# Optimization experiments

Hardware: AMD Instinct MI355X
Metric: run time of the kernel (lower is better)

## Reference

```python
import jax, jax.numpy as jnp
import numpy as np

N_EMBED = 512  # c in the original; scale uses sqrt(c), not head_size


def setup_inputs() -> dict:
    key = jax.random.key(0)
    k1, k2, k3, k4 = jax.random.split(key, 4)
    B, T, C, H = 4, 4096, N_EMBED, 64
    x = jax.random.normal(k1, (B, T, C), dtype=jnp.float32)
    Wk = jax.random.normal(k2, (C, H), dtype=jnp.float32) * (1.0 / np.sqrt(C))
    Wq = jax.random.normal(k3, (C, H), dtype=jnp.float32) * (1.0 / np.sqrt(C))
    Wv = jax.random.normal(k4, (C, H), dtype=jnp.float32) * (1.0 / np.sqrt(C))
    return {"x": x, "Wk": Wk, "Wq": Wq, "Wv": Wv}


def reference(x, Wk, Wq, Wv):
    # x: [B, T, C]; Wk/Wq/Wv: [C, H]
    B, T, C = x.shape
    k = jnp.einsum('btc,ch->bth', x, Wk)
    q = jnp.einsum('btc,ch->bth', x, Wq)
    v = jnp.einsum('btc,ch->bth', x, Wv)
    scale = 1.0 / jnp.sqrt(jnp.float32(C))  # original divides by sqrt(c)
    scores = jnp.einsum('bth,bsh->bts', q, k) * scale  # [B, T, T]
    causal = jnp.tril(jnp.ones((T, T), dtype=bool))
    scores = jnp.where(causal, scores, -jnp.inf)
    attn = jax.nn.softmax(scores, axis=-1)
    # dropout = 0.0 -> identity
    out = jnp.einsum('bts,bsh->bth', attn, v)  # [B, T, H]
    return out
```

## Files before the change

kernel.cpp:

```cpp
#include <hip/hip_runtime.h>
#include <hip/hip_bf16.h>
#include <math.h>

#define NB 4
#define NT 4096
#define NC 512
#define NH 64
#define KVBLK 64
#define LDK 72
#define MASKV (-1e30f)

typedef __attribute__((ext_vector_type(8))) short bf16x8;
typedef __attribute__((ext_vector_type(4))) float f32x4;

__device__ inline unsigned short f2bf(float f) {
    __hip_bfloat16 h = __float2bfloat16(f);
    return *reinterpret_cast<unsigned short*>(&h);
}

__global__ __launch_bounds__(256) void wconv(
    const float* __restrict__ Wk, const float* __restrict__ Wq,
    const float* __restrict__ Wv, unsigned short* __restrict__ Wt)
{
    int idx = blockIdx.x * 256 + threadIdx.x;
    int n = idx % 192, c = idx / 192;
    int sel = n >> 6, h = n & 63;
    const float* W = (sel == 0) ? Wq : (sel == 1) ? Wk : Wv;
    float val = W[c * NH + h];
    if (sel == 0) val *= 0.044194173824159216f;
    Wt[n * NC + c] = f2bf(val);
}

__global__ __launch_bounds__(256) void qkv_gemm(
    const float* __restrict__ x, const unsigned short* __restrict__ Wt,
    unsigned short* __restrict__ q, unsigned short* __restrict__ k,
    unsigned short* __restrict__ vt)
{
    __shared__ unsigned short xa[32][LDK];
    __shared__ unsigned short wb[192][LDK];

    const int tid = threadIdx.x;
    const int w = tid >> 6, lane = tid & 63, l15 = lane & 15, g = lane >> 4;
    const size_t r0 = (size_t)blockIdx.x * 32;

    f32x4 acc[2][3];
    #pragma unroll
    for (int mt = 0; mt < 2; ++mt)
        #pragma unroll
        for (int nt = 0; nt < 3; ++nt) acc[mt][nt] = (f32x4){0.f,0.f,0.f,0.f};

    for (int c0 = 0; c0 < NC; c0 += 64) {
        __syncthreads();
        {
            int row = tid >> 3, f8 = tid & 7;
            const float* xp = x + (r0 + row) * NC + c0 + f8*8;
            float4 x0 = *reinterpret_cast<const float4*>(xp);
            float4 x1 = *reinterpret_cast<const float4*>(xp + 4);
            bf16x8 a8;
            a8[0]=f2bf(x0.x); a8[1]=f2bf(x0.y); a8[2]=f2bf(x0.z); a8[3]=f2bf(x0.w);
            a8[4]=f2bf(x1.x); a8[5]=f2bf(x1.y); a8[6]=f2bf(x1.z); a8[7]=f2bf(x1.w);
            *reinterpret_cast<bf16x8*>(&xa[row][f8*8]) = a8;
        }
        #pragma unroll
        for (int i = 0; i < 6; ++i) {
            int idx = tid + 256*i;
            int row = idx >> 3, f8 = idx & 7;
            bf16x8 w8 = *reinterpret_cast<const bf16x8*>(Wt + (size_t)row * NC + c0 + f8*8);
            *reinterpret_cast<bf16x8*>(&wb[row][f8*8]) = w8;
        }
        __syncthreads();

        #pragma unroll
        for (int kk = 0; kk < 2; ++kk) {
            bf16x8 a[2], bfr[3];
            #pragma unroll
            for (int mt = 0; mt < 2; ++mt)
                a[mt] = *reinterpret_cast<const bf16x8*>(&xa[16*mt + l15][32*kk + 8*g]);
            #pragma unroll
            for (int nt = 0; nt < 3; ++nt)
                bfr[nt] = *reinterpret_cast<const bf16x8*>(&wb[48*w + 16*nt + l15][32*kk + 8*g]);
            __builtin_amdgcn_s_setprio(1);
            #pragma unroll
            for (int mt = 0; mt < 2; ++mt)
                #pragma unroll
                for (int nt = 0; nt < 3; ++nt)
                    acc[mt][nt] = __builtin_amdgcn_mfma_f32_16x16x32_bf16(a[mt], bfr[nt], acc[mt][nt], 0, 0, 0);
            __builtin_amdgcn_s_setprio(0);
        }
    }

    #pragma unroll
    for (int mt = 0; mt < 2; ++mt)
        #pragma unroll
        for (int nt = 0; nt < 3; ++nt) {
            int ncol = 48*w + 16*nt + l15;
            int sel = ncol >> 6, h = ncol & 63;
            if (sel < 2) {
                unsigned short* dst = (sel == 0) ? q : k;
                #pragma unroll
                for (int r = 0; r < 4; ++r)
                    dst[(r0 + 16*mt + 4*g + r) * NH + h] = f2bf(acc[mt][nt][r]);
            } else {
                int bb = (int)(r0 >> 12);
                int trow = ((int)r0 & (NT-1)) + 16*mt + 4*g;
                unsigned int lo = (unsigned int)f2bf(acc[mt][nt][0]) | ((unsigned int)f2bf(acc[mt][nt][1]) << 16);
                unsigned int hi = (unsigned int)f2bf(acc[mt][nt][2]) | ((unsigned int)f2bf(acc[mt][nt][3]) << 16);
                *reinterpret_cast<uint2*>(&vt[((size_t)bb*NH + h)*NT + trow]) = make_uint2(lo, hi);
            }
        }
}

__global__ __launch_bounds__(64, 3) void attn_part(
    const unsigned short* __restrict__ qg,
    const unsigned short* __restrict__ kg,
    const unsigned short* __restrict__ vtg,
    float* __restrict__ out,
    float* __restrict__ O_part,
    float* __restrict__ ML_part)
{
    const int qt = 127 - blockIdx.x;
    const int nT = (qt >> 1) + 1;
    const int ch = blockIdx.y;
    if (8 * ch >= nT) return;
    const int b  = blockIdx.z;

    __shared__ unsigned short p_lds[32][LDK];

    const int lane = threadIdx.x & 63;
    const int l15  = lane & 15;
    const int g    = lane >> 4;

    const int q0 = qt * 32;
    const size_t base = (size_t)b * NT * NH;

    bf16x8 qf[2][2];
    #pragma unroll
    for (int qc = 0; qc < 2; ++qc) {
        const unsigned short* qp = qg + base + (size_t)(q0 + 16*qc + l15) * NH + 8*g;
        qf[qc][0] = *reinterpret_cast<const bf16x8*>(qp);
        qf[qc][1] = *reinterpret_cast<const bf16x8*>(qp + 32);
    }

    f32x4 ot[4][2];
    #pragma unroll
    for (int dt = 0; dt < 4; ++dt)
        #pragma unroll
        for (int qc = 0; qc < 2; ++qc) ot[dt][qc] = (f32x4){0.f,0.f,0.f,0.f};
    float m0 = MASKV, m1 = MASKV, l0 = 0.f, l1 = 0.f;

    const int tBeg = 8 * ch;
    const int tEnd = min(8 * (ch + 1), nT);

    for (int it = tBeg; it < tEnd; ++it) {
        const int s0 = it * KVBLK;

        const unsigned short* kbase = kg + base + (size_t)(s0 + l15) * NH + 8*g;
        bf16x8 ka[4][2];
        #pragma unroll
        for (int t = 0; t < 4; ++t)
            #pragma unroll
            for (int kk = 0; kk < 2; ++kk)
                ka[t][kk] = *reinterpret_cast<const bf16x8*>(kbase + t*16*NH + kk*32);

        f32x4 s[4][2];
        __builtin_amdgcn_s_setprio(1);
        #pragma unroll
        for (int t = 0; t < 4; ++t)
            #pragma unroll
            for (int qc = 0; qc < 2; ++qc) {
                s[t][qc] = __builtin_amdgcn_mfma_f32_16x16x32_bf16(ka[t][0], qf[qc][0], (f32x4){0.f,0.f,0.f,0.f}, 0, 0, 0);
                s[t][qc] = __builtin_amdgcn_mfma_f32_16x16x32_bf16(ka[t][1], qf[qc][1], s[t][qc], 0, 0, 0);
            }
        __builtin_amdgcn_s_setprio(0);

        const unsigned short* vbase = vtg + ((size_t)b*NH + l15)*NT + s0 + 8*g;
        bf16x8 vf[4][2];
        #pragma unroll
        for (int dt = 0; dt < 4; ++dt)
            #pragma unroll
            for (int kk = 0; kk < 2; ++kk)
                vf[dt][kk] = *reinterpret_cast<const bf16x8*>(vbase + (size_t)dt*16*NT + kk*32);

        if (s0 + KVBLK - 1 > q0) {
            #pragma unroll
            for (int t = 0; t < 4; ++t)
                #pragma unroll
                for (int qc = 0; qc < 2; ++qc) {
                    const int qr = q0 + 16*qc + l15;
                    #pragma unroll
                    for (int r = 0; r < 4; ++r)
                        if (s0 + 16*t + 4*g + r > qr) s[t][qc][r] = MASKV;
                }
        }

        float pm0 = MASKV, pm1 = MASKV;
        #pragma unroll
        for (int t = 0; t < 4; ++t)
            #pragma unroll
            for (int r = 0; r < 4; ++r) {
                pm0 = fmaxf(pm0, s[t][0][r]);
                pm1 = fmaxf(pm1, s[t][1][r]);
            }
        pm0 = fmaxf(pm0, __shfl_xor(pm0, 16)); pm0 = fmaxf(pm0, __shfl_xor(pm0, 32));
        pm1 = fmaxf(pm1, __shfl_xor(pm1, 16)); pm1 = fmaxf(pm1, __shfl_xor(pm1, 32));

        if (!__all(pm0 <= m0 + 8.f && pm1 <= m1 + 8.f)) {
            float mn0 = fmaxf(m0, pm0), mn1 = fmaxf(m1, pm1);
            float c0 = __expf(m0 - mn0), c1 = __expf(m1 - mn1);
            l0 *= c0; l1 *= c1;
            #pragma unroll
            for (int dt = 0; dt < 4; ++dt)
                #pragma unroll
                for (int e = 0; e < 4; ++e) {
                    ot[dt][0][e] *= c0;
                    ot[dt][1][e] *= c1;
                }
            m0 = mn0; m1 = mn1;
        }

        float ps0 = 0.f, ps1 = 0.f;
        #pragma unroll
        for (int t = 0; t < 4; ++t)
            #pragma unroll
            for (int r = 0; r < 4; ++r) {
                float p0 = __expf(s[t][0][r] - m0);
                float p1 = __expf(s[t][1][r] - m1);
                s[t][0][r] = p0; s[t][1][r] = p1;
                ps0 += p0; ps1 += p1;
            }

        #pragma unroll
        for (int qc = 0; qc < 2; ++qc)
            #pragma unroll
            for (int t = 0; t < 4; ++t) {
                unsigned int w0 = (unsigned int)f2bf(s[t][qc][0]) | ((unsigned int)f2bf(s[t][qc][1]) << 16);
                unsigned int w1 = (unsigned int)f2bf(s[t][qc][2]) | ((unsigned int)f2bf(s[t][qc][3]) << 16);
                *reinterpret_cast<unsigned int*>(&p_lds[16*qc + l15][16*t + 4*g])     = w0;
                *reinterpret_cast<unsigned int*>(&p_lds[16*qc + l15][16*t + 4*g + 2]) = w1;
            }

        ps0 += __shfl_xor(ps0, 16); ps0 += __shfl_xor(ps0, 32);
        ps1 += __shfl_xor(ps1, 16); ps1 += __shfl_xor(ps1, 32);
        l0 += ps0; l1 += ps1;

        bf16x8 pf[2][2];
        #pragma unroll
        for (int qc = 0; qc < 2; ++qc)
            #pragma unroll
            for (int kk = 0; kk < 2; ++kk)
                pf[qc][kk] = *reinterpret_cast<const bf16x8*>(&p_lds[16*qc + l15][8*g + 32*kk]);
        __builtin_amdgcn_s_setprio(1);
        #pragma unroll
        for (int kk = 0; kk < 2; ++kk)
            #pragma unroll
            for (int dt = 0; dt < 4; ++dt)
                #pragma unroll
                for (int qc = 0; qc < 2; ++qc)
                    ot[dt][qc] = __builtin_amdgcn_mfma_f32_16x16x32_bf16(vf[dt][kk], pf[qc][kk], ot[dt][qc], 0, 0, 0);
        __builtin_amdgcn_s_setprio(0);
    }

    if (nT <= 8) {
        const float inv0 = 1.f / l0, inv1 = 1.f / l1;
        #pragma unroll
        for (int qc = 0; qc < 2; ++qc) {
            float inv = qc ? inv1 : inv0;
            float* orow = out + base + (size_t)(q0 + 16*qc + l15) * NH;
            #pragma unroll
            for (int dt = 0; dt < 4; ++dt) {
                f32x4 o4;
                #pragma unroll
                for (int r = 0; r < 4; ++r) o4[r] = ot[dt][qc][r] * inv;
                *reinterpret_cast<f32x4*>(&orow[16*dt + 4*g]) = o4;
            }
        }
    } else {
        const int slot = ((b * 128 + qt) << 3) + ch;
        float* op = O_part + (size_t)slot * (32*NH);
        #pragma unroll
        for (int qc = 0; qc < 2; ++qc)
            #pragma unroll
            for (int dt = 0; dt < 4; ++dt)
                *reinterpret_cast<f32x4*>(&op[(size_t)(16*qc + l15) * NH + 16*dt + 4*g]) = ot[dt][qc];
        if (g == 0) {
            float* mlp = ML_part + (size_t)slot * 64;
            *reinterpret_cast<float2*>(&mlp[2*l15])        = make_float2(m0, l0);
            *reinterpret_cast<float2*>(&mlp[2*(16 + l15)]) = make_float2(m1, l1);
        }
    }
}

__global__ __launch_bounds__(256) void attn_merge(
    const float* __restrict__ O_part,
    const float* __restrict__ ML_part,
    float* __restrict__ out)
{
    const int qt = 16 + blockIdx.x;
    const int b  = blockIdx.y;
    const int nch = (((qt >> 1) + 1) + 7) >> 3;
    const int slot0 = ((b * 128 + qt) << 3);
    const int row = threadIdx.x >> 3;
    const int dq  = (threadIdx.x & 7) * 8;

    float M = MASKV;
    for (int c = 0; c < nch; ++c)
        M = fmaxf(M, ML_part[(size_t)(slot0 + c) * 64 + 2*row]);

    float L = 0.f;
    float acc[8];
    #pragma unroll
    for (int j = 0; j < 8; ++j) acc[j] = 0.f;

    for (int c = 0; c < nch; ++c) {
        const float* mlp = &ML_part[(size_t)(slot0 + c) * 64 + 2*row];
        float wgt = __expf(mlp[0] - M);
        L += wgt * mlp[1];
        const float* op = O_part + (size_t)(slot0 + c) * (32*NH) + (size_t)row * NH + dq;
        #pragma unroll
        for (int j4 = 0; j4 < 2; ++j4) {
            float4 o4 = *reinterpret_cast<const float4*>(op + 4*j4);
            acc[4*j4+0] = fmaf(wgt, o4.x, acc[4*j4+0]);
            acc[4*j4+1] = fmaf(wgt, o4.y, acc[4*j4+1]);
            acc[4*j4+2] = fmaf(wgt, o4.z, acc[4*j4+2]);
            acc[4*j4+3] = fmaf(wgt, o4.w, acc[4*j4+3]);
        }
    }

    const float inv = 1.f / L;
    float* orow = out + (size_t)b * NT * NH + (size_t)(qt * 32 + row) * NH + dq;
    #pragma unroll
    for (int j4 = 0; j4 < 2; ++j4) {
        float4 o4;
        o4.x = acc[4*j4+0] * inv;
        o4.y = acc[4*j4+1] * inv;
        o4.z = acc[4*j4+2] * inv;
        o4.w = acc[4*j4+3] * inv;
        *reinterpret_cast<float4*>(orow + 4*j4) = o4;
    }
}

extern "C" void kernel_launch(void* const* d_in, const int* in_sizes, int n_in,
                              void* d_out, int out_size, void* d_ws, size_t ws_size,
                              hipStream_t stream) {
    const float* x  = (const float*)d_in[0];
    const float* Wk = (const float*)d_in[1];
    const float* Wq = (const float*)d_in[2];
    const float* Wv = (const float*)d_in[3];
    float* out = (float*)d_out;

    const size_t n = (size_t)NB * NT * NH;
    unsigned short* qb = (unsigned short*)d_ws;
    unsigned short* kb = qb + n;
    unsigned short* vt = kb + n;
    unsigned short* Wt = vt + n;
    float* O_part  = (float*)(Wt + 192 * NC);
    float* ML_part = O_part + (size_t)4096 * 32 * NH;

    wconv<<<(192*NC)/256, 256, 0, stream>>>(Wk, Wq, Wv, Wt);
    qkv_gemm<<<(NB*NT)/32, 256, 0, stream>>>(x, Wt, qb, kb, vt);

    dim3 pgrid(128, 8, NB);
    attn_part<<<pgrid, 64, 0, stream>>>(qb, kb, vt, out, O_part, ML_part);
    dim3 mgrid(112, NB);
    attn_merge<<<mgrid, 256, 0, stream>>>(O_part, ML_part, out);
}
```

Baseline: 73.76 us.

## Split KV into finer chunks, pack four waves per block, store bf16 partials

The KV range per split shrinks from 8 tiles to 4, and four independent wave-level work items are packed into each 256-thread block, so the work is spread across more waves with better occupancy. The softmax switches to exp2f, with log2(e) folded into the Q scaling. Partial outputs are stored as bf16 instead of fp32 to cut merge-pass traffic. The cost is more partials to merge and reduced precision in the partial accumulators. Waves whose chunk index is out of range exit early, which leaves some lanes in a block idle.

```diff
diff --git a/kernel.cpp b/kernel.cpp
--- a/kernel.cpp
+++ b/kernel.cpp
@@ -9,6 +9,7 @@
 #define KVBLK 64
 #define LDK 72
 #define MASKV (-1e30f)
+#define CHT 4
 
 typedef __attribute__((ext_vector_type(8))) short bf16x8;
 typedef __attribute__((ext_vector_type(4))) float f32x4;
@@ -16,6 +17,10 @@
 __device__ inline unsigned short f2bf(float f) {
     __hip_bfloat16 h = __float2bfloat16(f);
     return *reinterpret_cast<unsigned short*>(&h);
+}
+__device__ inline float bf2f(unsigned int u16bits) {
+    unsigned int u = u16bits << 16;
+    return *reinterpret_cast<float*>(&u);
 }
 
 __global__ __launch_bounds__(256) void wconv(
@@ -27,7 +32,7 @@
     int sel = n >> 6, h = n & 63;
     const float* W = (sel == 0) ? Wq : (sel == 1) ? Wk : Wv;
     float val = W[c * NH + h];
-    if (sel == 0) val *= 0.044194173824159216f;
+    if (sel == 0) val *= 0.063758715f;
     Wt[n * NC + c] = f2bf(val);
 }
 
@@ -110,26 +115,27 @@
         }
 }
 
-__global__ __launch_bounds__(64, 3) void attn_part(
+__global__ __launch_bounds__(256, 4) void attn_part(
     const unsigned short* __restrict__ qg,
     const unsigned short* __restrict__ kg,
     const unsigned short* __restrict__ vtg,
     float* __restrict__ out,
-    float* __restrict__ O_part,
+    unsigned short* __restrict__ O_part,
     float* __restrict__ ML_part)
 {
-    const int qt = 127 - blockIdx.x;
+    __shared__ unsigned short p_lds[4][32][LDK];
+
+    const int w    = threadIdx.x >> 6;
+    const int lane = threadIdx.x & 63;
+    const int linear = blockIdx.x * 4 + w;
+    const int ch = linear & 15;
+    const int qt = 127 - (linear >> 4);
     const int nT = (qt >> 1) + 1;
-    const int ch = blockIdx.y;
-    if (8 * ch >= nT) return;
-    const int b  = blockIdx.z;
-
-    __shared__ unsigned short p_lds[32][LDK];
-
-    const int lane = threadIdx.x & 63;
+    if (CHT * ch >= nT) return;
+    const int b  = blockIdx.y;
+
     const int l15  = lane & 15;
     const int g    = lane >> 4;
-
     const int q0 = qt * 32;
     const size_t base = (size_t)b * NT * NH;
 
@@ -148,8 +154,8 @@
         for (int qc = 0; qc < 2; ++qc) ot[dt][qc] = (f32x4){0.f,0.f,0.f,0.f};
     float m0 = MASKV, m1 = MASKV, l0 = 0.f, l1 = 0.f;
 
-    const int tBeg = 8 * ch;
-    const int tEnd = min(8 * (ch + 1), nT);
+    const int tBeg = CHT * ch;
+    const int tEnd = min(CHT * (ch + 1), nT);
 
     for (int it = tBeg; it < tEnd; ++it) {
         const int s0 = it * KVBLK;
@@ -206,7 +212,7 @@
 
         if (!__all(pm0 <= m0 + 8.f && pm1 <= m1 + 8.f)) {
             float mn0 = fmaxf(m0, pm0), mn1 = fmaxf(m1, pm1);
-            float c0 = __expf(m0 - mn0), c1 = __expf(m1 - mn1);
+            float c0 = exp2f(m0 - mn0), c1 = exp2f(m1 - mn1);
             l0 *= c0; l1 *= c1;
             #pragma unroll
             for (int dt = 0; dt < 4; ++dt)
@@ -223,8 +229,8 @@
         for (int t = 0; t < 4; ++t)
             #pragma unroll
             for (int r = 0; r < 4; ++r) {
-                float p0 = __expf(s[t][0][r] - m0);
-                float p1 = __expf(s[t][1][r] - m1);
+                float p0 = exp2f(s[t][0][r] - m0);
+                float p1 = exp2f(s[t][1][r] - m1);
                 s[t][0][r] = p0; s[t][1][r] = p1;
                 ps0 += p0; ps1 += p1;
             }
@@ -235,8 +241,8 @@
             for (int t = 0; t < 4; ++t) {
                 unsigned int w0 = (unsigned int)f2bf(s[t][qc][0]) | ((unsigned int)f2bf(s[t][qc][1]) << 16);
                 unsigned int w1 = (unsigned int)f2bf(s[t][qc][2]) | ((unsigned int)f2bf(s[t][qc][3]) << 16);
-                *reinterpret_cast<unsigned int*>(&p_lds[16*qc + l15][16*t + 4*g])     = w0;
-                *reinterpret_cast<unsigned int*>(&p_lds[16*qc + l15][16*t + 4*g + 2]) = w1;
+                *reinterpret_cast<unsigned int*>(&p_lds[w][16*qc + l15][16*t + 4*g])     = w0;
+                *reinterpret_cast<unsigned int*>(&p_lds[w][16*qc + l15][16*t + 4*g + 2]) = w1;
             }
 
         ps0 += __shfl_xor(ps0, 16); ps0 += __shfl_xor(ps0, 32);
@@ -248,7 +254,7 @@
         for (int qc = 0; qc < 2; ++qc)
             #pragma unroll
             for (int kk = 0; kk < 2; ++kk)
-                pf[qc][kk] = *reinterpret_cast<const bf16x8*>(&p_lds[16*qc + l15][8*g + 32*kk]);
+                pf[qc][kk] = *reinterpret_cast<const bf16x8*>(&p_lds[w][16*qc + l15][8*g + 32*kk]);
         __builtin_amdgcn_s_setprio(1);
         #pragma unroll
         for (int kk = 0; kk < 2; ++kk)
@@ -260,7 +266,7 @@
         __builtin_amdgcn_s_setprio(0);
     }
 
-    if (nT <= 8) {
+    if (nT <= CHT) {
         const float inv0 = 1.f / l0, inv1 = 1.f / l1;
         #pragma unroll
         for (int qc = 0; qc < 2; ++qc) {
@@ -275,13 +281,16 @@
             }
         }
     } else {
-        const int slot = ((b * 128 + qt) << 3) + ch;
-        float* op = O_part + (size_t)slot * (32*NH);
+        const int slot = ((b << 7 | qt) << 4) + ch;
+        unsigned short* op = O_part + (size_t)slot * (32*NH);
         #pragma unroll
         for (int qc = 0; qc < 2; ++qc)
             #pragma unroll
-            for (int dt = 0; dt < 4; ++dt)
-                *reinterpret_cast<f32x4*>(&op[(size_t)(16*qc + l15) * NH + 16*dt + 4*g]) = ot[dt][qc];
+            for (int dt = 0; dt < 4; ++dt) {
+                unsigned int lo = (unsigned int)f2bf(ot[dt][qc][0]) | ((unsigned int)f2bf(ot[dt][qc][1]) << 16);
+                unsigned int hi = (unsigned int)f2bf(ot[dt][qc][2]) | ((unsigned int)f2bf(ot[dt][qc][3]) << 16);
+                *reinterpret_cast<uint2*>(&op[(size_t)(16*qc + l15) * NH + 16*dt + 4*g]) = make_uint2(lo, hi);
+            }
         if (g == 0) {
             float* mlp = ML_part + (size_t)slot * 64;
             *reinterpret_cast<float2*>(&mlp[2*l15])        = make_float2(m0, l0);
@@ -291,14 +300,14 @@
 }
 
 __global__ __launch_bounds__(256) void attn_merge(
-    const float* __restrict__ O_part,
+    const unsigned short* __restrict__ O_part,
     const float* __restrict__ ML_part,
     float* __restrict__ out)
 {
-    const int qt = 16 + blockIdx.x;
+    const int qt = 8 + blockIdx.x;
     const int b  = blockIdx.y;
-    const int nch = (((qt >> 1) + 1) + 7) >> 3;
-    const int slot0 = ((b * 128 + qt) << 3);
+    const int nch = (((qt >> 1) + 1) + CHT - 1) / CHT;
+    const int slot0 = (b << 7 | qt) << 4;
     const int row = threadIdx.x >> 3;
     const int dq  = (threadIdx.x & 7) * 8;
 
@@ -313,17 +322,18 @@
 
     for (int c = 0; c < nch; ++c) {
         const float* mlp = &ML_part[(size_t)(slot0 + c) * 64 + 2*row];
-        float wgt = __expf(mlp[0] - M);
+        float wgt = exp2f(mlp[0] - M);
         L += wgt * mlp[1];
-        const float* op = O_part + (size_t)(slot0 + c) * (32*NH) + (size_t)row * NH + dq;
-        #pragma unroll
-        for (int j4 = 0; j4 < 2; ++j4) {
-            float4 o4 = *reinterpret_cast<const float4*>(op + 4*j4);
-            acc[4*j4+0] = fmaf(wgt, o4.x, acc[4*j4+0]);
-            acc[4*j4+1] = fmaf(wgt, o4.y, acc[4*j4+1]);
-            acc[4*j4+2] = fmaf(wgt, o4.z, acc[4*j4+2]);
-            acc[4*j4+3] = fmaf(wgt, o4.w, acc[4*j4+3]);
-        }
+        const unsigned short* op = O_part + (size_t)(slot0 + c) * (32*NH) + (size_t)row * NH + dq;
+        uint4 pk = *reinterpret_cast<const uint4*>(op);
+        acc[0] = fmaf(wgt, bf2f(pk.x & 0xffff), acc[0]);
+        acc[1] = fmaf(wgt, bf2f(pk.x >> 16),    acc[1]);
+        acc[2] = fmaf(wgt, bf2f(pk.y & 0xffff), acc[2]);
+        acc[3] = fmaf(wgt, bf2f(pk.y >> 16),    acc[3]);
+        acc[4] = fmaf(wgt, bf2f(pk.z & 0xffff), acc[4]);
+        acc[5] = fmaf(wgt, bf2f(pk.z >> 16),    acc[5]);
+        acc[6] = fmaf(wgt, bf2f(pk.w & 0xffff), acc[6]);
+        acc[7] = fmaf(wgt, bf2f(pk.w >> 16),    acc[7]);
     }
 
     const float inv = 1.f / L;
@@ -353,14 +363,14 @@
     unsigned short* kb = qb + n;
     unsigned short* vt = kb + n;
     unsigned short* Wt = vt + n;
-    float* O_part  = (float*)(Wt + 192 * NC);
-    float* ML_part = O_part + (size_t)4096 * 32 * NH;
+    unsigned short* O_part = Wt + 192 * NC;
+    float* ML_part = (float*)(O_part + (size_t)8192 * 32 * NH);
 
     wconv<<<(192*NC)/256, 256, 0, stream>>>(Wk, Wq, Wv, Wt);
     qkv_gemm<<<(NB*NT)/32, 256, 0, stream>>>(x, Wt, qb, kb, vt);
 
-    dim3 pgrid(128, 8, NB);
-    attn_part<<<pgrid, 64, 0, stream>>>(qb, kb, vt, out, O_part, ML_part);
-    dim3 mgrid(112, NB);
+    dim3 pgrid(512, NB);
+    attn_part<<<pgrid, 256, 0, stream>>>(qb, kb, vt, out, O_part, ML_part);
+    dim3 mgrid(120, NB);
     attn_merge<<<mgrid, 256, 0, stream>>>(O_part, ML_part, out);
 }
```

Measured after the change: 127.2 us. 72.4% more time.
